# Performance work log

Measured on AMD Instinct MI355X. Metric: run time of the kernel, lower is better.

Reference implementation:

```python
import jax, jax.numpy as jnp
import numpy as np

B, L, DM = 16, 1024, 128
DK = DV = 32
HF, HG, HC, HP, HT, HA = 2, 2, 2, 2, 1, 2  # full, log, local, prob, FFT, auto heads
MA = 25          # series_decomp moving average window
WIN = 32         # local attention causal window
EPS = 1e-5
SCALE = float(1.0 / np.sqrt(DK))

_i = np.arange(L)[:, None]
_j = np.arange(L)[None, :]
_d = _i - _j
# log-sparse: attend to self and keys at power-of-two causal distances
LOG_MASK = jnp.asarray((_d == 0) | ((_d > 0) & ((_d & (_d - 1)) == 0)))
LOC_MASK = jnp.asarray((_d >= 0) & (_d < WIN))
# ProbSparse (Informer, factor=5): fixed sample indices, u = U_part
_U = min(int(5 * np.ceil(np.log(L))), L)
PROB_IDX = jnp.asarray(np.random.RandomState(0).randint(0, L, size=(L, _U)))
AUTO_K = int(np.log(L))  # AutoCorrelation factor=1


def _cconv(x, w, b, pad):
    # x [B,L,DM] -> conv over time in NCH layout; pad-left = causal (Conv pad=2 + Chomp1d(2))
    y = jax.lax.conv_general_dilated(x.swapaxes(1, 2), w, (1,), [(pad, 0)],
                                     dimension_numbers=('NCH', 'OIH', 'NCH'))
    return y + b[None, :, None]


def _heads(y, H, d):
    # faithful to torch: .view(B, L, H, d) applied to [B, C, L] conv output (memory reinterpret)
    return y.reshape(y.shape[0], L, H, d)


def _qkv(xq, xk, xv, wq, bq, wk, bk, wv, bv, H):
    Q = _heads(_cconv(xq, wq, bq, 2), H, DK)
    K = _heads(_cconv(xk, wk, bk, 2), H, DK)
    V = _heads(_cconv(xv, wv, bv, 0), H, DV)
    return Q, K, V


def _attn(Q, K, V, mask=None):
    s = jnp.einsum('blhe,bshe->bhls', Q, K) * SCALE
    if mask is not None:
        s = jnp.where(mask, s, -1e9)
    return jnp.einsum('bhls,bshd->blhd', jax.nn.softmax(s, axis=-1), V)


def _prob_attn(Q, K, V):
    q, k, v = Q.swapaxes(1, 2), K.swapaxes(1, 2), V.swapaxes(1, 2)  # [B,H,L,D]
    Ks = k[:, :, PROB_IDX]                                  # [B,H,L,U,D] sampled keys
    qk = jnp.einsum('bhld,bhlud->bhlu', q, Ks)
    M = qk.max(-1) - qk.sum(-1) / L                         # sparsity measure
    top = jax.lax.top_k(M, _U)[1]                           # [B,H,u] active queries
    qr = jnp.take_along_axis(q, top[..., None], axis=2)
    sc = jnp.einsum('bhud,bhsd->bhus', qr, k) * SCALE
    cu = jnp.einsum('bhus,bhsd->bhud', jax.nn.softmax(sc, -1), v)
    ctx = jnp.broadcast_to(v.mean(axis=2, keepdims=True), v.shape)  # lazy queries get mean(V)
    bi = jnp.arange(v.shape[0])[:, None, None]
    hi = jnp.arange(v.shape[1])[None, :, None]
    return ctx.at[bi, hi, top].set(cu).swapaxes(1, 2)


def _auto_corr(Q, K, V):
    q = Q.transpose(0, 2, 3, 1)  # [B,H,E,L]
    k = K.transpose(0, 2, 3, 1)
    v = V.transpose(0, 2, 3, 1)
    corr = jnp.fft.irfft(jnp.fft.rfft(q, axis=-1) * jnp.conj(jnp.fft.rfft(k, axis=-1)), n=L, axis=-1)
    mv = corr.mean(axis=1).mean(axis=1)                     # [B,L] mean over heads+channels
    idx = jax.lax.top_k(mv.mean(axis=0), AUTO_K)[1]         # shared top-k delays
    w = jax.nn.softmax(mv[:, idx], axis=-1)                 # [B,k]
    tt = jnp.arange(L)
    agg = jnp.zeros_like(v)
    for i in range(AUTO_K):
        agg = agg + v[..., (tt + idx[i]) % L] * w[:, i][:, None, None, None]
    return agg.transpose(0, 3, 1, 2)                        # [B,L,H,E]


def _mavg(x, k):
    # replicate-padded moving average (Autoformer series_decomp) via cumsum
    p = (k - 1) // 2
    xp = jnp.concatenate([jnp.repeat(x[:, :1], p, axis=1), x, jnp.repeat(x[:, -1:], p, axis=1)], axis=1)
    cs = jnp.cumsum(xp, axis=1)
    cs = jnp.concatenate([jnp.zeros_like(cs[:, :1]), cs], axis=1)
    return (cs[:, k:] - cs[:, :-k]) / k


def _forward(fl):
    (iq, ik, iv,
     wqf, bqf, wkf, bkf, wvf, bvf,
     wqg, bqg, wkg, bkg, wvg, bvg,
     wql, bql, wkl, bkl, wvl, bvl,
     wqp, bqp, wkp, bkp, wvp, bvp,
     wqa, bqa, wka, bka, wva, bva,
     wfft, bfft, wap, bap, was, bas, wfc) = fl
    ctx = []
    Q, K, V = _qkv(iq, ik, iv, wqf, bqf, wkf, bkf, wvf, bvf, HF)
    ctx.append(_attn(Q, K, V))
    Q, K, V = _qkv(iq, ik, iv, wqg, bqg, wkg, bkg, wvg, bvg, HG)
    ctx.append(_attn(Q, K, V, LOG_MASK))
    Q, K, V = _qkv(iq, ik, iv, wql, bql, wkl, bkl, wvl, bvl, HC)
    ctx.append(_attn(Q, K, V, LOC_MASK))
    Q, K, V = _qkv(iq, ik, iv, wqp, bqp, wkp, bkp, wvp, bvp, HP)
    ctx.append(_prob_attn(Q, K, V))
    cf = jnp.fft.fft(iq, axis=1).real                       # FFT branch
    ctx.append((cf @ wfft + bfft).reshape(B, L, HT, DV))
    Q, K, V = _qkv(iq, ik, iv, wqa, bqa, wka, bka, wva, bva, HA)
    ca = _auto_corr(Q, K, V).reshape(B, L, HA * DV) @ wap + bap
    ca = iq + ca                                            # residual (dropout=eval identity)
    ca = ca - _mavg(ca, MA)                                 # seasonal part of series_decomp
    ctx.append((ca @ was + bas).reshape(B, L, HA, DV))
    c = jnp.concatenate(ctx, axis=2).reshape(B, L, -1)
    out = c @ wfc + iq
    mu = out.mean(-1, keepdims=True)
    var = out.var(-1, keepdims=True)                        # fresh LayerNorm: weight=1, bias=0
    return (out - mu) / jnp.sqrt(var + EPS)


def setup_inputs() -> dict:
    ks = iter(jax.random.split(jax.random.key(0), 64))
    def n(shape, s=0.02):
        return jax.random.normal(next(ks), shape, dtype=jnp.float32) * s
    d = {}
    d['input_Q'] = jax.random.normal(next(ks), (B, L, DM), dtype=jnp.float32)
    d['input_K'] = jax.random.normal(next(ks), (B, L, DM), dtype=jnp.float32)
    d['input_V'] = jax.random.normal(next(ks), (B, L, DM), dtype=jnp.float32)
    for nm, H in [('full', HF), ('log', HG), ('loc', HC), ('prob', HP), ('auto', HA)]:
        d['wq_' + nm] = n((DK * H, DM, 3)); d['bq_' + nm] = n((DK * H,))
        d['wk_' + nm] = n((DK * H, DM, 3)); d['bk_' + nm] = n((DK * H,))
        d['wv_' + nm] = n((DV * H, DM, 1)); d['bv_' + nm] = n((DV * H,))
    d['w_fft'] = n((DM, DV * HT)); d['b_fft'] = n((DV * HT,))
    d['w_aproj'] = n((DV * HA, DM)); d['b_aproj'] = n((DM,))
    d['w_asize'] = n((DM, DV * HA)); d['b_asize'] = n((DV * HA,))
    d['w_fc'] = n(((HF + HG + HC + HP + HT + HA) * DV, DM))
    return d


def reference(input_Q, input_K, input_V, wq_full, bq_full, wk_full, bk_full, wv_full, bv_full, wq_log, bq_log, wk_log, bk_log, wv_log, bv_log, wq_loc, bq_loc, wk_loc, bk_loc, wv_loc, bv_loc, wq_prob, bq_prob, wk_prob, bk_prob, wv_prob, bv_prob, wq_auto, bq_auto, wk_auto, bk_auto, wv_auto, bv_auto, w_fft, b_fft, w_aproj, b_aproj, w_asize, b_asize, w_fc):
    return _forward((input_Q, input_K, input_V, wq_full, bq_full, wk_full, bk_full, wv_full, bv_full, wq_log, bq_log, wk_log, bk_log, wv_log, bv_log, wq_loc, bq_loc, wk_loc, bk_loc, wv_loc, bv_loc, wq_prob, bq_prob, wk_prob, bk_prob, wv_prob, bv_prob, wq_auto, bq_auto, wk_auto, bk_auto, wv_auto, bv_auto, w_fft, b_fft, w_aproj, b_aproj, w_asize, b_asize, w_fc))
```

## Files before the change

### kernel.cpp

```cpp
#include <hip/hip_runtime.h>
#include <hip/hip_bf16.h>
#include <math.h>

#define B_   16
#define L_   1024
#define SCALE_ 0.17677669529663687f

__global__ void mt_kernel(int* __restrict__ pidx) {
  __shared__ unsigned int mt[624];
  int tid = threadIdx.x;
  if (tid == 0) {
    unsigned int s = 0u;
    for (int i = 0; i < 624; ++i) {
      mt[i] = s;
      s = 1812433253u * (s ^ (s >> 30)) + (unsigned)(i + 1);
    }
  }
  __syncthreads();
  const unsigned int HI = 0x80000000u, LO = 0x7fffffffu, MM = 0x9908b0dfu;
  for (int blk = 0; blk < 58; ++blk) {
    unsigned int n0 = 0, n1 = 0, n2 = 0, old623 = 0;
    bool a0 = tid < 227, a2 = tid < 169;
    if (a0) {
      unsigned int y0 = (mt[tid] & HI) | (mt[tid + 1] & LO);
      n0 = mt[tid + 397] ^ (y0 >> 1) ^ ((y0 & 1u) ? MM : 0u);
      unsigned int y1 = (mt[tid + 227] & HI) | (mt[tid + 228] & LO);
      n1 = n0 ^ (y1 >> 1) ^ ((y1 & 1u) ? MM : 0u);
      if (a2) {
        unsigned int y2 = (mt[tid + 454] & HI) | (mt[tid + 455] & LO);
        n2 = n1 ^ (y2 >> 1) ^ ((y2 & 1u) ? MM : 0u);
      }
      if (tid == 169) old623 = mt[623];
    }
    __syncthreads();
    if (a0) {
      mt[tid] = n0;
      mt[tid + 227] = n1;
      if (a2) mt[tid + 454] = n2;
    }
    __syncthreads();
    if (tid == 169) {
      unsigned int y = (old623 & HI) | (mt[0] & LO);
      mt[623] = n1 ^ (y >> 1) ^ ((y & 1u) ? MM : 0u);
    }
    __syncthreads();
    for (int i = tid; i < 624; i += 256) {
      int g = blk * 624 + i;
      if (g < 35840) {
        unsigned int y = mt[i];
        y ^= y >> 11;
        y ^= (y << 7) & 0x9d2c5680u;
        y ^= (y << 15) & 0xefc60000u;
        y ^= y >> 18;
        pidx[g] = (int)(y & 1023u);
      }
    }
  }
}

__device__ __forceinline__ void conv_body(const float* __restrict__ x,
                                          const float* __restrict__ w,
                                          const float* __restrict__ bias,
                                          float* __restrict__ out,
                                          float* smem, int b, int t0, int tid, int is1) {
  int c = tid & 63, tt0 = (tid >> 6) * 8;
  float acc[8];
  float bvv = bias[c];
  #pragma unroll
  for (int j = 0; j < 8; ++j) acc[j] = bvv;
  if (!is1) {
    float* xs = smem;
    float* ws = smem + 4352;
    for (int i = tid; i < 34 * 128; i += 256) {
      int r = i >> 7, d = i & 127;
      int t = t0 - 2 + r;
      xs[r * 128 + d] = (t >= 0) ? x[(size_t)b * 131072 + (size_t)t * 128 + d] : 0.0f;
    }
    for (int dc = 0; dc < 128; dc += 16) {
      __syncthreads();
      {
        int row = tid >> 2, sub = tid & 3;
        const float* wsrc = w + row * 384 + dc * 3 + sub * 12;
        float* wdst = ws + row * 49 + sub * 12;
        #pragma unroll
        for (int k = 0; k < 12; ++k) wdst[k] = wsrc[k];
      }
      __syncthreads();
      #pragma unroll
      for (int dl = 0; dl < 16; dl += 4) {
        int d0 = dc + dl;
        float4 xr[10];
        #pragma unroll
        for (int r = 0; r < 10; ++r) xr[r] = *(const float4*)&xs[(tt0 + r) * 128 + d0];
        float wreg[12];
        #pragma unroll
        for (int jj = 0; jj < 12; ++jj) wreg[jj] = ws[c * 49 + dl * 3 + jj];
        #pragma unroll
        for (int j = 0; j < 8; ++j) {
          float a = acc[j];
          #pragma unroll
          for (int k = 0; k < 3; ++k) {
            float4 xv4 = xr[j + k];
            a = fmaf(wreg[0 + k], xv4.x, a);
            a = fmaf(wreg[3 + k], xv4.y, a);
            a = fmaf(wreg[6 + k], xv4.z, a);
            a = fmaf(wreg[9 + k], xv4.w, a);
          }
          acc[j] = a;
        }
      }
    }
  } else {
    float* xs = smem;
    float* ws = smem + 4096;
    for (int i = tid; i < 32 * 128; i += 256) {
      int r = i >> 7, d = i & 127;
      xs[r * 128 + d] = x[(size_t)b * 131072 + (size_t)(t0 + r) * 128 + d];
    }
    for (int dc = 0; dc < 128; dc += 32) {
      __syncthreads();
      {
        int row = tid >> 2, sub = tid & 3;
        const float* wsrc = w + row * 128 + dc + sub * 8;
        float* wdst = ws + row * 33 + sub * 8;
        #pragma unroll
        for (int k = 0; k < 8; ++k) wdst[k] = wsrc[k];
      }
      __syncthreads();
      #pragma unroll
      for (int dl = 0; dl < 32; dl += 4) {
        int d0 = dc + dl;
        float w0 = ws[c * 33 + dl], w1 = ws[c * 33 + dl + 1];
        float w2 = ws[c * 33 + dl + 2], w3 = ws[c * 33 + dl + 3];
        #pragma unroll
        for (int j = 0; j < 8; ++j) {
          float4 xv4 = *(const float4*)&xs[(tt0 + j) * 128 + d0];
          float a = acc[j];
          a = fmaf(w0, xv4.x, a);
          a = fmaf(w1, xv4.y, a);
          a = fmaf(w2, xv4.z, a);
          a = fmaf(w3, xv4.w, a);
          acc[j] = a;
        }
      }
    }
  }
  float* op = out + (size_t)b * 65536 + (size_t)c * 1024 + t0 + tt0;
  #pragma unroll
  for (int j = 0; j < 8; ++j) op[j] = acc[j];
}

__global__ __launch_bounds__(256, 4)
void qkv_conv_kernel(const float* __restrict__ xq, const float* __restrict__ xk,
                     const float* __restrict__ xv,
                     const float* __restrict__ wq, const float* __restrict__ bq,
                     const float* __restrict__ wk, const float* __restrict__ bk,
                     const float* __restrict__ wv, const float* __restrict__ bv,
                     float* __restrict__ qo, float* __restrict__ ko,
                     float* __restrict__ vo) {
  __shared__ float smem[7488];
  int which = blockIdx.z;
  const float* x = (which == 0) ? xq : (which == 1) ? xk : xv;
  const float* w = (which == 0) ? wq : (which == 1) ? wk : wv;
  const float* bias = (which == 0) ? bq : (which == 1) ? bk : bv;
  float* out = (which == 0) ? qo : (which == 1) ? ko : vo;
  conv_body(x, w, bias, out, smem, blockIdx.y, blockIdx.x * 32, threadIdx.x, which == 2);
}

struct ConvArgs {
  const float* x[3];
  const float* w[15];
  const float* bia[15];
  float* outbase;
};
__global__ __launch_bounds__(256, 4)
void qkv_conv_all(ConvArgs a) {
  __shared__ float smem[7488];
  int z = blockIdx.z;
  int which = z % 3;
  float* out = a.outbase + (size_t)z * 1048576;
  conv_body(a.x[which], a.w[z], a.bia[z], out, smem, blockIdx.y, blockIdx.x * 32,
            threadIdx.x, which == 2);
}

__global__ __launch_bounds__(256, 2)
void attn_full_part(const float* __restrict__ Q, const float* __restrict__ K,
                    const float* __restrict__ V, float* __restrict__ part,
                    int stile, int nstage) {
  __shared__ float Ks[128][32];
  __shared__ float Vs[128][32];
  int bh = blockIdx.z, b = bh >> 1, h = bh & 1;
  int l = blockIdx.x * 256 + threadIdx.x;
  int s0 = blockIdx.y * stile;
  const float* Kb = K + (size_t)b * 65536 + h * 32;
  const float* Vb = V + (size_t)b * 65536 + h * 32;
  const float* Qb = Q + (size_t)b * 65536 + h * 32 + (size_t)l * 64;
  float q[32];
  #pragma unroll
  for (int i = 0; i < 8; ++i) {
    float4 v4 = ((const float4*)Qb)[i];
    q[4*i] = v4.x; q[4*i+1] = v4.y; q[4*i+2] = v4.z; q[4*i+3] = v4.w;
  }
  float o[32];
  #pragma unroll
  for (int d = 0; d < 32; ++d) o[d] = 0.0f;
  float ssum = 0.0f;
  for (int st = 0; st < nstage; ++st) {
    __syncthreads();
    int sb = s0 + st * 128;
    for (int i = threadIdx.x; i < 1024; i += 256) {
      int r = i >> 3, d4 = i & 7;
      ((float4*)&Ks[r][0])[d4] = *(const float4*)(Kb + (size_t)(sb + r) * 64 + d4 * 4);
      ((float4*)&Vs[r][0])[d4] = *(const float4*)(Vb + (size_t)(sb + r) * 64 + d4 * 4);
    }
    __syncthreads();
    for (int s = 0; s < 128; s += 2) {
      const float4* kp0 = (const float4*)&Ks[s][0];
      const float4* kp1 = (const float4*)&Ks[s + 1][0];
      float a0 = 0, a1 = 0, a2 = 0, a3 = 0;
      float c0 = 0, c1 = 0, c2 = 0, c3 = 0;
      #pragma unroll
      for (int i = 0; i < 8; ++i) {
        float4 k0 = kp0[i], k1 = kp1[i];
        float qx = q[4*i], qy = q[4*i+1], qz = q[4*i+2], qw = q[4*i+3];
        a0 = fmaf(qx, k0.x, a0); a1 = fmaf(qy, k0.y, a1);
        a2 = fmaf(qz, k0.z, a2); a3 = fmaf(qw, k0.w, a3);
        c0 = fmaf(qx, k1.x, c0); c1 = fmaf(qy, k1.y, c1);
        c2 = fmaf(qz, k1.z, c2); c3 = fmaf(qw, k1.w, c3);
      }
      float p0 = __expf(((a0 + a1) + (a2 + a3)) * SCALE_);
      float p1 = __expf(((c0 + c1) + (c2 + c3)) * SCALE_);
      ssum += p0 + p1;
      const float4* vp0 = (const float4*)&Vs[s][0];
      const float4* vp1 = (const float4*)&Vs[s + 1][0];
      #pragma unroll
      for (int i = 0; i < 8; ++i) {
        float4 v0 = vp0[i], v1 = vp1[i];
        o[4*i]   = fmaf(p0, v0.x, fmaf(p1, v1.x, o[4*i]));
        o[4*i+1] = fmaf(p0, v0.y, fmaf(p1, v1.y, o[4*i+1]));
        o[4*i+2] = fmaf(p0, v0.z, fmaf(p1, v1.z, o[4*i+2]));
        o[4*i+3] = fmaf(p0, v0.w, fmaf(p1, v1.w, o[4*i+3]));
      }
    }
  }
  float* pp = part + (((size_t)bh * gridDim.y + blockIdx.y) * 1024 + l) * 36;
  #pragma unroll
  for (int i = 0; i < 8; ++i)
    ((float4*)pp)[i] = make_float4(o[4*i], o[4*i+1], o[4*i+2], o[4*i+3]);
  pp[32] = ssum;
}

__global__ void attn_full_comb(const float* __restrict__ part, float* __restrict__ cbuf,
                               int nsplit) {
  int idx = blockIdx.x * 128 + threadIdx.x;
  int bh = idx >> 10, l = idx & 1023;
  int b = bh >> 1, h = bh & 1;
  float S = 0.0f;
  float o[32];
  #pragma unroll
  for (int d = 0; d < 32; ++d) o[d] = 0.0f;
  for (int j = 0; j < nsplit; ++j) {
    const float* pp = part + (((size_t)bh * nsplit + j) * 1024 + l) * 36;
    S += pp[32];
    #pragma unroll
    for (int i = 0; i < 8; ++i) {
      float4 v4 = ((const float4*)pp)[i];
      o[4*i] += v4.x; o[4*i+1] += v4.y; o[4*i+2] += v4.z; o[4*i+3] += v4.w;
    }
  }
  float inv = 1.0f / S;
  float* cc = cbuf + ((size_t)b * 1024 + l) * 352 + 0 + h * 32;
  #pragma unroll
  for (int d = 0; d < 32; ++d) cc[d] = o[d] * inv;
}

__global__ void attn_log_kernel(const float* __restrict__ Q, const float* __restrict__ K,
                                const float* __restrict__ V, float* __restrict__ cbuf) {
  int idx = blockIdx.x * 128 + threadIdx.x;
  int bh = idx >> 10, l = idx & 1023;
  int b = bh >> 1, h = bh & 1;
  const float* Qb = Q + (size_t)b * 65536 + h * 32;
  const float* Kb = K + (size_t)b * 65536 + h * 32;
  const float* Vb = V + (size_t)b * 65536 + h * 32;
  float q[32];
  #pragma unroll
  for (int i = 0; i < 8; ++i) {
    float4 v4 = ((const float4*)(Qb + (size_t)l * 64))[i];
    q[4*i] = v4.x; q[4*i+1] = v4.y; q[4*i+2] = v4.z; q[4*i+3] = v4.w;
  }
  float o[32];
  #pragma unroll
  for (int d = 0; d < 32; ++d) o[d] = 0.0f;
  float ssum = 0.0f;
  #pragma unroll
  for (int j = 0; j < 11; ++j) {
    int off = (j == 0) ? 0 : (1 << (j - 1));
    if (off <= l) {
      int s = l - off;
      const float4* kp = (const float4*)(Kb + (size_t)s * 64);
      float a0 = 0, a1 = 0, a2 = 0, a3 = 0;
      #pragma unroll
      for (int i = 0; i < 8; ++i) {
        float4 kv = kp[i];
        a0 = fmaf(q[4*i], kv.x, a0);
        a1 = fmaf(q[4*i+1], kv.y, a1);
        a2 = fmaf(q[4*i+2], kv.z, a2);
        a3 = fmaf(q[4*i+3], kv.w, a3);
      }
      float p = __expf(((a0 + a1) + (a2 + a3)) * SCALE_);
      ssum += p;
      const float4* vp = (const float4*)(Vb + (size_t)s * 64);
      #pragma unroll
      for (int i = 0; i < 8; ++i) {
        float4 vv = vp[i];
        o[4*i]   = fmaf(p, vv.x, o[4*i]);
        o[4*i+1] = fmaf(p, vv.y, o[4*i+1]);
        o[4*i+2] = fmaf(p, vv.z, o[4*i+2]);
        o[4*i+3] = fmaf(p, vv.w, o[4*i+3]);
      }
    }
  }
  float inv = 1.0f / ssum;
  float* cc = cbuf + ((size_t)b * 1024 + l) * 352 + 64 + h * 32;
  #pragma unroll
  for (int d = 0; d < 32; ++d) cc[d] = o[d] * inv;
}

__global__ void attn_loc_kernel(const float* __restrict__ Q, const float* __restrict__ K,
                                const float* __restrict__ V, float* __restrict__ cbuf) {
  int idx = blockIdx.x * 128 + threadIdx.x;
  int bh = idx >> 10, l = idx & 1023;
  int b = bh >> 1, h = bh & 1;
  const float* Qb = Q + (size_t)b * 65536 + h * 32;
  const float* Kb = K + (size_t)b * 65536 + h * 32;
  const float* Vb = V + (size_t)b * 65536 + h * 32;
  float q[32];
  #pragma unroll
  for (int i = 0; i < 8; ++i) {
    float4 v4 = ((const float4*)(Qb + (size_t)l * 64))[i];
    q[4*i] = v4.x; q[4*i+1] = v4.y; q[4*i+2] = v4.z; q[4*i+3] = v4.w;
  }
  float o[32];
  #pragma unroll
  for (int d = 0; d < 32; ++d) o[d] = 0.0f;
  float ssum = 0.0f;
  int jlo = (l >= 31) ? 0 : (31 - l);
  for (int j = jlo; j < 32; ++j) {
    int s = l - 31 + j;
    const float4* kp = (const float4*)(Kb + (size_t)s * 64);
    float a0 = 0, a1 = 0, a2 = 0, a3 = 0;
    #pragma unroll
    for (int i = 0; i < 8; ++i) {
      float4 kv = kp[i];
      a0 = fmaf(q[4*i], kv.x, a0);
      a1 = fmaf(q[4*i+1], kv.y, a1);
      a2 = fmaf(q[4*i+2], kv.z, a2);
      a3 = fmaf(q[4*i+3], kv.w, a3);
    }
    float p = __expf(((a0 + a1) + (a2 + a3)) * SCALE_);
    ssum += p;
    const float4* vp = (const float4*)(Vb + (size_t)s * 64);
    #pragma unroll
    for (int i = 0; i < 8; ++i) {
      float4 vv = vp[i];
      o[4*i]   = fmaf(p, vv.x, o[4*i]);
      o[4*i+1] = fmaf(p, vv.y, o[4*i+1]);
      o[4*i+2] = fmaf(p, vv.z, o[4*i+2]);
      o[4*i+3] = fmaf(p, vv.w, o[4*i+3]);
    }
  }
  float inv = 1.0f / ssum;
  float* cc = cbuf + ((size_t)b * 1024 + l) * 352 + 128 + h * 32;
  #pragma unroll
  for (int d = 0; d < 32; ++d) cc[d] = o[d] * inv;
}

__global__ void prob_m_kernel(const float* __restrict__ Q, const float* __restrict__ K,
                              const int* __restrict__ pidx, float* __restrict__ Mbuf) {
  int idx = blockIdx.x * 128 + threadIdx.x;
  int bh = idx >> 10, l = idx & 1023;
  int b = bh >> 1, h = bh & 1;
  const float* Qb = Q + (size_t)b * 65536 + h * 32;
  const float* Kb = K + (size_t)b * 65536 + h * 32;
  float q[32];
  #pragma unroll
  for (int i = 0; i < 8; ++i) {
    float4 v4 = ((const float4*)(Qb + (size_t)l * 64))[i];
    q[4*i] = v4.x; q[4*i+1] = v4.y; q[4*i+2] = v4.z; q[4*i+3] = v4.w;
  }
  float mx = -1e30f, sm = 0.0f;
  for (int u = 0; u < 35; ++u) {
    int ki = pidx[l * 35 + u];
    const float4* kp = (const float4*)(Kb + (size_t)ki * 64);
    float a0 = 0, a1 = 0, a2 = 0, a3 = 0;
    #pragma unroll
    for (int i = 0; i < 8; ++i) {
      float4 kv = kp[i];
      a0 = fmaf(q[4*i], kv.x, a0);
      a1 = fmaf(q[4*i+1], kv.y, a1);
      a2 = fmaf(q[4*i+2], kv.z, a2);
      a3 = fmaf(q[4*i+3], kv.w, a3);
    }
    float s = (a0 + a1) + (a2 + a3);
    mx = fmaxf(mx, s);
    sm += s;
  }
  Mbuf[(size_t)bh * 1024 + l] = mx - sm * (1.0f / 1024.0f);
}

__global__ void top35_kernel(const float* __restrict__ Mbuf, int* __restrict__ sel) {
  int bh = blockIdx.x;
  int lane = threadIdx.x;
  float v[16];
  const float* Mb = Mbuf + (size_t)bh * 1024 + lane * 16;
  #pragma unroll
  for (int k = 0; k < 16; ++k) v[k] = Mb[k];
  for (int it = 0; it < 35; ++it) {
    float bv = -1e30f; int bi = 0;
    #pragma unroll
    for (int k = 0; k < 16; ++k)
      if (v[k] > bv) { bv = v[k]; bi = k; }
    int gidx = lane * 16 + bi;
    #pragma unroll
    for (int off = 32; off > 0; off >>= 1) {
      float ov = __shfl_down(bv, off, 64);
      int og = __shfl_down(gidx, off, 64);
      if (ov > bv || (ov == bv && og < gidx)) { bv = ov; gidx = og; }
    }
    gidx = __shfl(gidx, 0, 64);
    if (lane == 0) sel[bh * 35 + it] = gidx;
    if ((gidx >> 4) == lane) {
      int kk = gidx & 15;
      #pragma unroll
      for (int k = 0; k < 16; ++k)
        if (k == kk) v[k] = -1e30f;
    }
  }
}

__global__ void prob_fill_kernel(const float* __restrict__ V, float* __restrict__ cbuf) {
  __shared__ float red[256];
  __shared__ float vm[32];
  int bh = blockIdx.x, b = bh >> 1, h = bh & 1;
  int tid = threadIdx.x;
  int d = tid & 31, ch = tid >> 5;
  const float* Vb = V + (size_t)b * 65536 + h * 32;
  float s = 0.0f;
  for (int ss = ch * 128; ss < ch * 128 + 128; ++ss) s += Vb[(size_t)ss * 64 + d];
  red[tid] = s;
  __syncthreads();
  if (ch == 0) {
    float t = 0.0f;
    for (int c = 0; c < 8; ++c) t += red[c * 32 + d];
    vm[d] = t * (1.0f / 1024.0f);
  }
  __syncthreads();
  for (int i = tid; i < 1024 * 32; i += 256) {
    int l = i >> 5, dd = i & 31;
    cbuf[((size_t)b * 1024 + l) * 352 + 192 + h * 32 + dd] = vm[dd];
  }
}

__global__ void prob_part_kernel(const float* __restrict__ Q, const float* __restrict__ K,
                                 const float* __restrict__ V, const int* __restrict__ sel,
                                 float* __restrict__ ppart) {
  int bh = blockIdx.y, b = bh >> 1, h = bh & 1;
  int sc0 = blockIdx.x * 64;
  int u = threadIdx.x;
  int uu = (u < 35) ? u : 34;
  int l = sel[bh * 35 + uu];
  const float* Qb = Q + (size_t)b * 65536 + h * 32;
  const float* Kb = K + (size_t)b * 65536 + h * 32;
  const float* Vb = V + (size_t)b * 65536 + h * 32;
  float q[32];
  #pragma unroll
  for (int i = 0; i < 8; ++i) {
    float4 v4 = ((const float4*)(Qb + (size_t)l * 64))[i];
    q[4*i] = v4.x; q[4*i+1] = v4.y; q[4*i+2] = v4.z; q[4*i+3] = v4.w;
  }
  float o[32];
  #pragma unroll
  for (int dd = 0; dd < 32; ++dd) o[dd] = 0.0f;
  float ssum = 0.0f;
  for (int s = sc0; s < sc0 + 64; ++s) {
    const float4* kp = (const float4*)(Kb + (size_t)s * 64);
    float a0 = 0, a1 = 0, a2 = 0, a3 = 0;
    #pragma unroll
    for (int i = 0; i < 8; ++i) {
      float4 kv = kp[i];
      a0 = fmaf(q[4*i], kv.x, a0);
      a1 = fmaf(q[4*i+1], kv.y, a1);
      a2 = fmaf(q[4*i+2], kv.z, a2);
      a3 = fmaf(q[4*i+3], kv.w, a3);
    }
    float p = __expf(((a0 + a1) + (a2 + a3)) * SCALE_);
    ssum += p;
    const float4* vp = (const float4*)(Vb + (size_t)s * 64);
    #pragma unroll
    for (int i = 0; i < 8; ++i) {
      float4 vv = vp[i];
      o[4*i]   = fmaf(p, vv.x, o[4*i]);
      o[4*i+1] = fmaf(p, vv.y, o[4*i+1]);
      o[4*i+2] = fmaf(p, vv.z, o[4*i+2]);
      o[4*i+3] = fmaf(p, vv.w, o[4*i+3]);
    }
  }
  if (u < 35) {
    float* pp = ppart + (((size_t)bh * 16 + blockIdx.x) * 35 + u) * 36;
    #pragma unroll
    for (int i = 0; i < 8; ++i)
      ((float4*)pp)[i] = make_float4(o[4*i], o[4*i+1], o[4*i+2], o[4*i+3]);
    pp[32] = ssum;
  }
}

__global__ void prob_comb_kernel(const float* __restrict__ ppart, const int* __restrict__ sel,
                                 float* __restrict__ cbuf) {
  int t = blockIdx.x * 64 + threadIdx.x;
  if (t >= 32 * 35) return;
  int bh = t / 35, u = t % 35;
  int b = bh >> 1, h = bh & 1;
  int l = sel[bh * 35 + u];
  float S = 0.0f;
  float o[32];
  #pragma unroll
  for (int d = 0; d < 32; ++d) o[d] = 0.0f;
  for (int j = 0; j < 16; ++j) {
    const float* pp = ppart + (((size_t)bh * 16 + j) * 35 + u) * 36;
    S += pp[32];
    #pragma unroll
    for (int i = 0; i < 8; ++i) {
      float4 v4 = ((const float4*)pp)[i];
      o[4*i] += v4.x; o[4*i+1] += v4.y; o[4*i+2] += v4.z; o[4*i+3] += v4.w;
    }
  }
  float inv = 1.0f / S;
  float* cc = cbuf + ((size_t)b * 1024 + l) * 352 + 192 + h * 32;
  #pragma unroll
  for (int d = 0; d < 32; ++d) cc[d] = o[d] * inv;
}

__global__ void auto_mv_part(const float* __restrict__ Qa, const float* __restrict__ Ka,
                             float* __restrict__ part) {
  __shared__ float qs[1280];
  int c = blockIdx.x, tq = blockIdx.y, b = blockIdx.z;
  int tid = threadIdx.x;
  int tau0 = tq * 256;
  const float* Qb = Qa + (size_t)b * 65536 + (size_t)c * 1024;
  const float* Kb = Ka + (size_t)b * 65536 + (size_t)c * 1024;
  for (int i = tid; i < 1280; i += 256) qs[i] = Qb[(tau0 + i) & 1023];
  __syncthreads();
  float a0 = 0, a1 = 0, a2 = 0, a3 = 0;
  for (int t = 0; t < 1024; t += 8) {
    float4 k0 = *(const float4*)(Kb + t);
    float4 k1 = *(const float4*)(Kb + t + 4);
    const float* qp = &qs[t + tid];
    a0 = fmaf(k0.x, qp[0], a0);
    a1 = fmaf(k0.y, qp[1], a1);
    a2 = fmaf(k0.z, qp[2], a2);
    a3 = fmaf(k0.w, qp[3], a3);
    a0 = fmaf(k1.x, qp[4], a0);
    a1 = fmaf(k1.y, qp[5], a1);
    a2 = fmaf(k1.z, qp[6], a2);
    a3 = fmaf(k1.w, qp[7], a3);
  }
  part[(((size_t)b * 64 + c) << 10) + tau0 + tid] = (a0 + a1) + (a2 + a3);
}

__global__ void auto_mv_reduce(const float* __restrict__ part, float* __restrict__ mv) {
  int idx = blockIdx.x * 256 + threadIdx.x;
  int b = idx >> 10, tau = idx & 1023;
  float s = 0.0f;
  for (int c = 0; c < 64; ++c) s += part[(((size_t)b * 64 + c) << 10) + tau];
  mv[(size_t)b * 1024 + tau] = s * (1.0f / 64.0f);
}

__global__ void auto_top6_kernel(const float* __restrict__ mv, int* __restrict__ idx6,
                                 float* __restrict__ w6) {
  __shared__ int id6s[6];
  int lane = threadIdx.x;
  float v[16];
  #pragma unroll
  for (int k = 0; k < 16; ++k) {
    int i = lane * 16 + k;
    float s = 0.0f;
    for (int b = 0; b < 16; ++b) s += mv[(size_t)b * 1024 + i];
    v[k] = s;
  }
  for (int it = 0; it < 6; ++it) {
    float bv = -1e30f; int bi = 0;
    #pragma unroll
    for (int k = 0; k < 16; ++k)
      if (v[k] > bv) { bv = v[k]; bi = k; }
    int gidx = lane * 16 + bi;
    #pragma unroll
    for (int off = 32; off > 0; off >>= 1) {
      float ov = __shfl_down(bv, off, 64);
      int og = __shfl_down(gidx, off, 64);
      if (ov > bv || (ov == bv && og < gidx)) { bv = ov; gidx = og; }
    }
    gidx = __shfl(gidx, 0, 64);
    if (lane == 0) { idx6[it] = gidx; id6s[it] = gidx; }
    if ((gidx >> 4) == lane) {
      int kk = gidx & 15;
      #pragma unroll
      for (int k = 0; k < 16; ++k)
        if (k == kk) v[k] = -1e30f;
    }
  }
  __syncthreads();
  if (lane < 16) {
    int b = lane;
    float vals[6]; float mx = -1e30f;
    #pragma unroll
    for (int j = 0; j < 6; ++j) { vals[j] = mv[(size_t)b * 1024 + id6s[j]]; mx = fmaxf(mx, vals[j]); }
    float s = 0.0f;
    #pragma unroll
    for (int j = 0; j < 6; ++j) { vals[j] = __expf(vals[j] - mx); s += vals[j]; }
    #pragma unroll
    for (int j = 0; j < 6; ++j) w6[b * 6 + j] = vals[j] / s;
  }
}

__global__ void auto_agg_kernel(const float* __restrict__ Va, const float* __restrict__ iq,
                                const float* __restrict__ wap, const float* __restrict__ bap,
                                const int* __restrict__ idx6, const float* __restrict__ w6,
                                float* __restrict__ ca) {
  __shared__ float aggs[16][64];
  __shared__ float w6s[6];
  __shared__ int id6[6];
  int b = blockIdx.y, t0 = blockIdx.x * 16;
  int tid = threadIdx.x;
  if (tid < 6) { w6s[tid] = w6[b * 6 + tid]; id6[tid] = idx6[tid]; }
  __syncthreads();
  const float* Vb = Va + (size_t)b * 65536;
  for (int i = tid; i < 1024; i += 256) {
    int tl = i >> 6, c = i & 63;
    int t = t0 + tl;
    float s = 0.0f;
    #pragma unroll
    for (int j = 0; j < 6; ++j)
      s += w6s[j] * Vb[(size_t)((t + id6[j]) & 1023) * 64 + c];
    aggs[tl][c] = s;
  }
  __syncthreads();
  int dm = tid & 127, tp = tid >> 7;
  float acc[8];
  #pragma unroll
  for (int r = 0; r < 8; ++r) {
    int t = t0 + tp * 8 + r;
    acc[r] = bap[dm] + iq[((size_t)b * 1024 + t) * 128 + dm];
  }
  for (int c = 0; c < 64; ++c) {
    float wv = wap[c * 128 + dm];
    #pragma unroll
    for (int r = 0; r < 8; ++r) acc[r] += aggs[tp * 8 + r][c] * wv;
  }
  #pragma unroll
  for (int r = 0; r < 8; ++r)
    ca[((size_t)b * 1024 + t0 + tp * 8 + r) * 128 + dm] = acc[r];
}

__global__ void auto_ma_kernel(const float* __restrict__ ca, const float* __restrict__ was,
                               const float* __restrict__ bas, float* __restrict__ cbuf) {
  __shared__ float cas[40][128];
  __shared__ float diff[16][128];
  int b = blockIdx.y, t0 = blockIdx.x * 16;
  int tid = threadIdx.x;
  for (int i = tid; i < 40 * 128; i += 256) {
    int r = i >> 7, d = i & 127;
    int t = t0 - 12 + r;
    t = (t < 0) ? 0 : ((t > 1023) ? 1023 : t);
    cas[r][d] = ca[((size_t)b * 1024 + t) * 128 + d];
  }
  __syncthreads();
  int d = tid & 127, hf = tid >> 7;
  int tl0 = hf * 8;
  float s = 0.0f;
  #pragma unroll
  for (int w = 0; w < 25; ++w) s += cas[tl0 + w][d];
  #pragma unroll
  for (int k = 0; k < 8; ++k) {
    int tl = tl0 + k;
    diff[tl][d] = cas[tl + 12][d] - s * (1.0f / 25.0f);
    if (k < 7) s += cas[tl + 25][d] - cas[tl][d];
  }
  __syncthreads();
  int j = tid & 63, tq = tid >> 6;
  float acc[4];
  #pragma unroll
  for (int r = 0; r < 4; ++r) acc[r] = bas[j];
  for (int dd = 0; dd < 128; ++dd) {
    float wv = was[dd * 64 + j];
    #pragma unroll
    for (int r = 0; r < 4; ++r) acc[r] += diff[tq * 4 + r][dd] * wv;
  }
  #pragma unroll
  for (int r = 0; r < 4; ++r)
    cbuf[((size_t)b * 1024 + t0 + tq * 4 + r) * 352 + 288 + j] = acc[r];
}

__global__ void fftY_kernel(const float* __restrict__ x, const float* __restrict__ wfft,
                            float* __restrict__ Y) {
  __shared__ float xs[64][128];
  __shared__ float ws[32][129];
  int b = blockIdx.y, t0 = blockIdx.x * 64;
  int tid = threadIdx.x;
  for (int i = tid; i < 64 * 128; i += 256) {
    int r = i >> 7, d = i & 127;
    xs[r][d] = x[(size_t)b * 131072 + (size_t)(t0 + r) * 128 + d];
  }
  for (int i = tid; i < 4096; i += 256) {
    int d = i >> 5, j = i & 31;
    ws[j][d] = wfft[i];
  }
  __syncthreads();
  int j = tid & 31, tt0 = (tid >> 5) * 8;
  float acc[8];
  #pragma unroll
  for (int r = 0; r < 8; ++r) acc[r] = 0.0f;
  for (int d0 = 0; d0 < 128; d0 += 4) {
    float w0 = ws[j][d0], w1 = ws[j][d0 + 1], w2 = ws[j][d0 + 2], w3 = ws[j][d0 + 3];
    #pragma unroll
    for (int r = 0; r < 8; ++r) {
      float4 xv = *(const float4*)&xs[tt0 + r][d0];
      float a = acc[r];
      a = fmaf(w0, xv.x, a);
      a = fmaf(w1, xv.y, a);
      a = fmaf(w2, xv.z, a);
      a = fmaf(w3, xv.w, a);
      acc[r] = a;
    }
  }
  #pragma unroll
  for (int r = 0; r < 8; ++r)
    Y[((size_t)b * 1024 + t0 + tt0 + r) * 32 + j] = acc[r];
}

__global__ void fftT_kernel(const float* __restrict__ Y, const float* __restrict__ bfft,
                            float* __restrict__ cbuf) {
  __shared__ float ys[256 * 32];
  __shared__ float altred[8][32];
  int b = blockIdx.y, fbase = blockIdx.x * 64;
  int tid = threadIdx.x;
  int fi = tid & 31, jg = tid >> 5, j0 = jg * 4;
  int f0 = fbase + fi * 2;
  const float TWO_PI_N = 6.283185307179586476925f / 1024.0f;
  float ca0, sa0, ca1, sa1;
  sincosf(TWO_PI_N * (float)f0, &sa0, &ca0);
  sincosf(TWO_PI_N * (float)(f0 + 1), &sa1, &ca1);
  float cr0 = 1.0f, ci0 = 0.0f, cr1 = 1.0f, ci1 = 0.0f;
  float4 acc0 = make_float4(0.f, 0.f, 0.f, 0.f);
  float4 acc1 = make_float4(0.f, 0.f, 0.f, 0.f);
  bool do512 = (blockIdx.x == 0);
  int aj = tid & 31, arow = tid >> 5;
  float alt = 0.0f;
  for (int chk = 0; chk < 4; ++chk) {
    __syncthreads();
    const float4* Yp = (const float4*)(Y + ((size_t)b * 1024 + chk * 256) * 32);
    for (int i = tid; i < 2048; i += 256) ((float4*)ys)[i] = Yp[i];
    __syncthreads();
    for (int tl = 0; tl < 256; ++tl) {
      float4 yv = *(const float4*)&ys[tl * 32 + j0];
      acc0.x = fmaf(cr0, yv.x, acc0.x);
      acc0.y = fmaf(cr0, yv.y, acc0.y);
      acc0.z = fmaf(cr0, yv.z, acc0.z);
      acc0.w = fmaf(cr0, yv.w, acc0.w);
      acc1.x = fmaf(cr1, yv.x, acc1.x);
      acc1.y = fmaf(cr1, yv.y, acc1.y);
      acc1.z = fmaf(cr1, yv.z, acc1.z);
      acc1.w = fmaf(cr1, yv.w, acc1.w);
      float nr0 = cr0 * ca0 - ci0 * sa0;
      float ni0 = cr0 * sa0 + ci0 * ca0;
      cr0 = nr0; ci0 = ni0;
      float nr1 = cr1 * ca1 - ci1 * sa1;
      float ni1 = cr1 * sa1 + ci1 * ca1;
      cr1 = nr1; ci1 = ni1;
    }
    if (do512) {
      int tb = arow * 32;
      #pragma unroll 8
      for (int k = 0; k < 32; ++k) {
        float y = ys[(tb + k) * 32 + aj];
        alt += ((tb + k) & 1) ? -y : y;
      }
    }
  }
  float b0 = bfft[j0], b1 = bfft[j0 + 1], b2 = bfft[j0 + 2], b3 = bfft[j0 + 3];
  float* cc0 = cbuf + ((size_t)b * 1024 + f0) * 352 + 256 + j0;
  cc0[0] = acc0.x + b0; cc0[1] = acc0.y + b1; cc0[2] = acc0.z + b2; cc0[3] = acc0.w + b3;
  float* cc1 = cbuf + ((size_t)b * 1024 + f0 + 1) * 352 + 256 + j0;
  cc1[0] = acc1.x + b0; cc1[1] = acc1.y + b1; cc1[2] = acc1.z + b2; cc1[3] = acc1.w + b3;
  if (f0 > 0) {
    float* cm0 = cbuf + ((size_t)b * 1024 + (1024 - f0)) * 352 + 256 + j0;
    cm0[0] = acc0.x + b0; cm0[1] = acc0.y + b1; cm0[2] = acc0.z + b2; cm0[3] = acc0.w + b3;
  }
  {
    float* cm1 = cbuf + ((size_t)b * 1024 + (1024 - f0 - 1)) * 352 + 256 + j0;
    cm1[0] = acc1.x + b0; cm1[1] = acc1.y + b1; cm1[2] = acc1.z + b2; cm1[3] = acc1.w + b3;
  }
  if (do512) {
    altred[arow][aj] = alt;
    __syncthreads();
    if (tid < 32) {
      float s = 0.0f;
      #pragma unroll
      for (int r = 0; r < 8; ++r) s += altred[r][tid];
      cbuf[((size_t)b * 1024 + 512) * 352 + 256 + tid] = s + bfft[tid];
    }
  }
}

__global__ void fc_ln_kernel(const float* __restrict__ cbuf, const float* __restrict__ wfc,
                             const float* __restrict__ iq, float* __restrict__ out) {
  __shared__ float cs[16][352];
  __shared__ float os[16][128];
  int b = blockIdx.y, t0 = blockIdx.x * 16;
  int tid = threadIdx.x;
  for (int i = tid; i < 16 * 352; i += 256) {
    int r = i / 352, col = i % 352;
    cs[r][col] = cbuf[((size_t)b * 1024 + t0 + r) * 352 + col];
  }
  __syncthreads();
  int j = tid & 127, half = tid >> 7;
  float acc[8];
  #pragma unroll
  for (int k = 0; k < 8; ++k)
    acc[k] = iq[((size_t)b * 1024 + t0 + half * 8 + k) * 128 + j];
  for (int i = 0; i < 352; ++i) {
    float wv = wfc[i * 128 + j];
    #pragma unroll
    for (int k = 0; k < 8; ++k) acc[k] += cs[half * 8 + k][i] * wv;
  }
  #pragma unroll
  for (int k = 0; k < 8; ++k) os[half * 8 + k][j] = acc[k];
  __syncthreads();
  int wid = tid >> 6, lane = tid & 63;
  for (int rr = 0; rr < 4; ++rr) {
    int r = wid * 4 + rr;
    float x0 = os[r][lane], x1 = os[r][lane + 64];
    float s1 = x0 + x1;
    float s2 = x0 * x0 + x1 * x1;
    #pragma unroll
    for (int k = 32; k > 0; k >>= 1) {
      s1 += __shfl_xor(s1, k, 64);
      s2 += __shfl_xor(s2, k, 64);
    }
    float mean = s1 * (1.0f / 128.0f);
    float var = s2 * (1.0f / 128.0f) - mean * mean;
    float rstd = 1.0f / sqrtf(var + 1e-5f);
    float* op = out + ((size_t)b * 1024 + t0 + r) * 128;
    op[lane] = (x0 - mean) * rstd;
    op[lane + 64] = (x1 - mean) * rstd;
  }
}

extern "C" void kernel_launch(void* const* d_in, const int* in_sizes, int n_in,
                              void* d_out, int out_size, void* d_ws, size_t ws_size,
                              hipStream_t stream) {
  (void)in_sizes; (void)n_in; (void)out_size;
  const float* inQ = (const float*)d_in[0];
  const float* inK = (const float*)d_in[1];
  const float* inV = (const float*)d_in[2];
  const float *wq[5], *bq[5], *wk[5], *bk[5], *wv[5], *bv[5];
  for (int br = 0; br < 5; ++br) {
    wq[br] = (const float*)d_in[3 + br * 6 + 0];
    bq[br] = (const float*)d_in[3 + br * 6 + 1];
    wk[br] = (const float*)d_in[3 + br * 6 + 2];
    bk[br] = (const float*)d_in[3 + br * 6 + 3];
    wv[br] = (const float*)d_in[3 + br * 6 + 4];
    bv[br] = (const float*)d_in[3 + br * 6 + 5];
  }
  const float* wfft = (const float*)d_in[33];
  const float* bfft = (const float*)d_in[34];
  const float* wap  = (const float*)d_in[35];
  const float* bap  = (const float*)d_in[36];
  const float* was  = (const float*)d_in[37];
  const float* bas  = (const float*)d_in[38];
  const float* wfc  = (const float*)d_in[39];
  float* out = (float*)d_out;

  bool mega = ws_size >= (size_t)128 * 1024 * 1024;
  int nsplit = (ws_size >= (size_t)76 * 1024 * 1024) ? 8 : 4;
  int stile = 1024 / nsplit;
  int nstage = stile / 128;

  char* wsb = (char*)d_ws;
  size_t off = 0;
  auto alloc = [&](size_t bytes) -> void* {
    void* p = wsb + off;
    off += (bytes + 255) & ~(size_t)255;
    return p;
  };
  int*   pidx = (int*)  alloc((size_t)35840 * 4);
  float* qkvall = (float*)alloc((size_t)(mega ? 15 : 3) * 1048576 * 4);
  float* cbuf = (float*)alloc((size_t)16 * 1024 * 352 * 4);
  float* fpart = (float*)alloc((size_t)32 * nsplit * 1024 * 36 * 4);
  float* Mbuf = (float*)alloc((size_t)32 * 1024 * 4);
  int*   sel  = (int*)  alloc((size_t)32 * 35 * 4);
  float* mvb  = (float*)alloc((size_t)16 * 1024 * 4);
  int*   idx6 = (int*)  alloc(64);
  float* w6   = (float*)alloc((size_t)16 * 6 * 4);
  float* ppart = fpart;
  float* cab   = fpart;
  float* mpart = (float*)((char*)fpart + (size_t)8 * 1024 * 1024);
  float* Ybuf  = (float*)((char*)fpart + (size_t)12 * 1024 * 1024);

  mt_kernel<<<1, 256, 0, stream>>>(pidx);

  if (mega) {
    ConvArgs ca;
    ca.x[0] = inQ; ca.x[1] = inK; ca.x[2] = inV;
    for (int br = 0; br < 5; ++br) {
      ca.w[br * 3 + 0] = wq[br]; ca.bia[br * 3 + 0] = bq[br];
      ca.w[br * 3 + 1] = wk[br]; ca.bia[br * 3 + 1] = bk[br];
      ca.w[br * 3 + 2] = wv[br]; ca.bia[br * 3 + 2] = bv[br];
    }
    ca.outbase = qkvall;
    qkv_conv_all<<<dim3(32, 16, 15), 256, 0, stream>>>(ca);
  }
  auto bufs = [&](int br, float*& qb, float*& kb, float*& vb) {
    int bi = mega ? br : 0;
    qb = qkvall + (size_t)(bi * 3 + 0) * 1048576;
    kb = qkvall + (size_t)(bi * 3 + 1) * 1048576;
    vb = qkvall + (size_t)(bi * 3 + 2) * 1048576;
  };
  auto conv_branch = [&](int br, float* qb, float* kb, float* vb) {
    if (!mega)
      qkv_conv_kernel<<<dim3(32, 16, 3), 256, 0, stream>>>(
          inQ, inK, inV, wq[br], bq[br], wk[br], bk[br], wv[br], bv[br], qb, kb, vb);
  };
  float *qb, *kb, *vb;

  bufs(0, qb, kb, vb);
  conv_branch(0, qb, kb, vb);
  attn_full_part<<<dim3(4, nsplit, 32), 256, 0, stream>>>(qb, kb, vb, fpart, stile, nstage);
  attn_full_comb<<<256, 128, 0, stream>>>(fpart, cbuf, nsplit);

  bufs(1, qb, kb, vb);
  conv_branch(1, qb, kb, vb);
  attn_log_kernel<<<256, 128, 0, stream>>>(qb, kb, vb, cbuf);

  bufs(2, qb, kb, vb);
  conv_branch(2, qb, kb, vb);
  attn_loc_kernel<<<256, 128, 0, stream>>>(qb, kb, vb, cbuf);

  bufs(3, qb, kb, vb);
  conv_branch(3, qb, kb, vb);
  prob_m_kernel<<<256, 128, 0, stream>>>(qb, kb, pidx, Mbuf);
  top35_kernel<<<32, 64, 0, stream>>>(Mbuf, sel);
  prob_fill_kernel<<<32, 256, 0, stream>>>(vb, cbuf);
  prob_part_kernel<<<dim3(16, 32), 64, 0, stream>>>(qb, kb, vb, sel, ppart);
  prob_comb_kernel<<<18, 64, 0, stream>>>(ppart, sel, cbuf);

  bufs(4, qb, kb, vb);
  conv_branch(4, qb, kb, vb);
  auto_mv_part<<<dim3(64, 4, 16), 256, 0, stream>>>(qb, kb, mpart);
  auto_mv_reduce<<<64, 256, 0, stream>>>(mpart, mvb);
  auto_top6_kernel<<<1, 64, 0, stream>>>(mvb, idx6, w6);
  auto_agg_kernel<<<dim3(64, 16), 256, 0, stream>>>(vb, inQ, wap, bap, idx6, w6, cab);
  auto_ma_kernel<<<dim3(64, 16), 256, 0, stream>>>(cab, was, bas, cbuf);

  fftY_kernel<<<dim3(16, 16), 256, 0, stream>>>(inQ, wfft, Ybuf);
  fftT_kernel<<<dim3(8, 16), 256, 0, stream>>>(Ybuf, bfft, cbuf);

  fc_ln_kernel<<<dim3(64, 16), 256, 0, stream>>>(cbuf, wfc, inQ, out);
}
```

Baseline: 764.5 us.

## Enlarge conv register tile to two channels and 64 timesteps per block

The causal QKV convolution now has each thread compute two output channels (cp and cp+32) for 8 timesteps, and each block covers 64 timesteps instead of 32. Every x value loaded from shared memory is reused for twice as many FMAs. Weights are read as float4 with a padded stride, outputs are written as float4, and the grid is halved along time. The larger shared tile and doubled accumulators lower the occupancy target from 4 to 3 blocks per CU and leave fewer blocks in the grid.

```diff
diff --git a/kernel.cpp b/kernel.cpp
--- a/kernel.cpp
+++ b/kernel.cpp
@@ -63,15 +63,17 @@
                                           const float* __restrict__ bias,
                                           float* __restrict__ out,
                                           float* smem, int b, int t0, int tid, int is1) {
-  int c = tid & 63, tt0 = (tid >> 6) * 8;
-  float acc[8];
-  float bvv = bias[c];
-  #pragma unroll
-  for (int j = 0; j < 8; ++j) acc[j] = bvv;
+  int cp = tid & 31;
+  int tg = tid >> 5;
+  int tt0 = tg * 8;
+  float acc0[8], acc1[8];
+  float b0v = bias[cp], b1v = bias[cp + 32];
+  #pragma unroll
+  for (int j = 0; j < 8; ++j) { acc0[j] = b0v; acc1[j] = b1v; }
   if (!is1) {
     float* xs = smem;
-    float* ws = smem + 4352;
-    for (int i = tid; i < 34 * 128; i += 256) {
+    float* ws = smem + 8448;
+    for (int i = tid; i < 66 * 128; i += 256) {
       int r = i >> 7, d = i & 127;
       int t = t0 - 2 + r;
       xs[r * 128 + d] = (t >= 0) ? x[(size_t)b * 131072 + (size_t)t * 128 + d] : 0.0f;
@@ -81,7 +83,7 @@
       {
         int row = tid >> 2, sub = tid & 3;
         const float* wsrc = w + row * 384 + dc * 3 + sub * 12;
-        float* wdst = ws + row * 49 + sub * 12;
+        float* wdst = ws + row * 52 + sub * 12;
         #pragma unroll
         for (int k = 0; k < 12; ++k) wdst[k] = wsrc[k];
       }
@@ -92,28 +94,39 @@
         float4 xr[10];
         #pragma unroll
         for (int r = 0; r < 10; ++r) xr[r] = *(const float4*)&xs[(tt0 + r) * 128 + d0];
-        float wreg[12];
-        #pragma unroll
-        for (int jj = 0; jj < 12; ++jj) wreg[jj] = ws[c * 49 + dl * 3 + jj];
+        float4 wa0 = *(const float4*)&ws[cp * 52 + dl * 3];
+        float4 wa1 = *(const float4*)&ws[cp * 52 + dl * 3 + 4];
+        float4 wa2 = *(const float4*)&ws[cp * 52 + dl * 3 + 8];
+        float4 wb0 = *(const float4*)&ws[(cp + 32) * 52 + dl * 3];
+        float4 wb1 = *(const float4*)&ws[(cp + 32) * 52 + dl * 3 + 4];
+        float4 wb2 = *(const float4*)&ws[(cp + 32) * 52 + dl * 3 + 8];
+        float w0r[12] = {wa0.x, wa0.y, wa0.z, wa0.w, wa1.x, wa1.y, wa1.z, wa1.w,
+                         wa2.x, wa2.y, wa2.z, wa2.w};
+        float w1r[12] = {wb0.x, wb0.y, wb0.z, wb0.w, wb1.x, wb1.y, wb1.z, wb1.w,
+                         wb2.x, wb2.y, wb2.z, wb2.w};
         #pragma unroll
         for (int j = 0; j < 8; ++j) {
-          float a = acc[j];
+          float a0 = acc0[j], a1 = acc1[j];
           #pragma unroll
           for (int k = 0; k < 3; ++k) {
-            float4 xv4 = xr[j + k];
-            a = fmaf(wreg[0 + k], xv4.x, a);
-            a = fmaf(wreg[3 + k], xv4.y, a);
-            a = fmaf(wreg[6 + k], xv4.z, a);
-            a = fmaf(wreg[9 + k], xv4.w, a);
+            float4 xv = xr[j + k];
+            a0 = fmaf(w0r[0 + k], xv.x, a0);
+            a0 = fmaf(w0r[3 + k], xv.y, a0);
+            a0 = fmaf(w0r[6 + k], xv.z, a0);
+            a0 = fmaf(w0r[9 + k], xv.w, a0);
+            a1 = fmaf(w1r[0 + k], xv.x, a1);
+            a1 = fmaf(w1r[3 + k], xv.y, a1);
+            a1 = fmaf(w1r[6 + k], xv.z, a1);
+            a1 = fmaf(w1r[9 + k], xv.w, a1);
           }
-          acc[j] = a;
+          acc0[j] = a0; acc1[j] = a1;
         }
       }
     }
   } else {
     float* xs = smem;
-    float* ws = smem + 4096;
-    for (int i = tid; i < 32 * 128; i += 256) {
+    float* ws = smem + 8192;
+    for (int i = tid; i < 64 * 128; i += 256) {
       int r = i >> 7, d = i & 127;
       xs[r * 128 + d] = x[(size_t)b * 131072 + (size_t)(t0 + r) * 128 + d];
     }
@@ -122,7 +135,7 @@
       {
         int row = tid >> 2, sub = tid & 3;
         const float* wsrc = w + row * 128 + dc + sub * 8;
-        float* wdst = ws + row * 33 + sub * 8;
+        float* wdst = ws + row * 36 + sub * 8;
         #pragma unroll
         for (int k = 0; k < 8; ++k) wdst[k] = wsrc[k];
       }
@@ -130,27 +143,34 @@
       #pragma unroll
       for (int dl = 0; dl < 32; dl += 4) {
         int d0 = dc + dl;
-        float w0 = ws[c * 33 + dl], w1 = ws[c * 33 + dl + 1];
-        float w2 = ws[c * 33 + dl + 2], w3 = ws[c * 33 + dl + 3];
+        float4 wv0 = *(const float4*)&ws[cp * 36 + dl];
+        float4 wv1 = *(const float4*)&ws[(cp + 32) * 36 + dl];
         #pragma unroll
         for (int j = 0; j < 8; ++j) {
-          float4 xv4 = *(const float4*)&xs[(tt0 + j) * 128 + d0];
-          float a = acc[j];
-          a = fmaf(w0, xv4.x, a);
-          a = fmaf(w1, xv4.y, a);
-          a = fmaf(w2, xv4.z, a);
-          a = fmaf(w3, xv4.w, a);
-          acc[j] = a;
+          float4 xv = *(const float4*)&xs[(tt0 + j) * 128 + d0];
+          float a0 = acc0[j], a1 = acc1[j];
+          a0 = fmaf(wv0.x, xv.x, a0);
+          a0 = fmaf(wv0.y, xv.y, a0);
+          a0 = fmaf(wv0.z, xv.z, a0);
+          a0 = fmaf(wv0.w, xv.w, a0);
+          a1 = fmaf(wv1.x, xv.x, a1);
+          a1 = fmaf(wv1.y, xv.y, a1);
+          a1 = fmaf(wv1.z, xv.z, a1);
+          a1 = fmaf(wv1.w, xv.w, a1);
+          acc0[j] = a0; acc1[j] = a1;
         }
       }
     }
   }
-  float* op = out + (size_t)b * 65536 + (size_t)c * 1024 + t0 + tt0;
-  #pragma unroll
-  for (int j = 0; j < 8; ++j) op[j] = acc[j];
-}
-
-__global__ __launch_bounds__(256, 4)
+  float* op0 = out + (size_t)b * 65536 + (size_t)cp * 1024 + t0 + tt0;
+  float* op1 = out + (size_t)b * 65536 + (size_t)(cp + 32) * 1024 + t0 + tt0;
+  *(float4*)op0 = make_float4(acc0[0], acc0[1], acc0[2], acc0[3]);
+  *(float4*)(op0 + 4) = make_float4(acc0[4], acc0[5], acc0[6], acc0[7]);
+  *(float4*)op1 = make_float4(acc1[0], acc1[1], acc1[2], acc1[3]);
+  *(float4*)(op1 + 4) = make_float4(acc1[4], acc1[5], acc1[6], acc1[7]);
+}
+
+__global__ __launch_bounds__(256, 3)
 void qkv_conv_kernel(const float* __restrict__ xq, const float* __restrict__ xk,
                      const float* __restrict__ xv,
                      const float* __restrict__ wq, const float* __restrict__ bq,
@@ -158,13 +178,13 @@
                      const float* __restrict__ wv, const float* __restrict__ bv,
                      float* __restrict__ qo, float* __restrict__ ko,
                      float* __restrict__ vo) {
-  __shared__ float smem[7488];
+  __shared__ float smem[11776];
   int which = blockIdx.z;
   const float* x = (which == 0) ? xq : (which == 1) ? xk : xv;
   const float* w = (which == 0) ? wq : (which == 1) ? wk : wv;
   const float* bias = (which == 0) ? bq : (which == 1) ? bk : bv;
   float* out = (which == 0) ? qo : (which == 1) ? ko : vo;
-  conv_body(x, w, bias, out, smem, blockIdx.y, blockIdx.x * 32, threadIdx.x, which == 2);
+  conv_body(x, w, bias, out, smem, blockIdx.y, blockIdx.x * 64, threadIdx.x, which == 2);
 }
 
 struct ConvArgs {
@@ -173,13 +193,13 @@
   const float* bia[15];
   float* outbase;
 };
-__global__ __launch_bounds__(256, 4)
+__global__ __launch_bounds__(256, 3)
 void qkv_conv_all(ConvArgs a) {
-  __shared__ float smem[7488];
+  __shared__ float smem[11776];
   int z = blockIdx.z;
   int which = z % 3;
   float* out = a.outbase + (size_t)z * 1048576;
-  conv_body(a.x[which], a.w[z], a.bia[z], out, smem, blockIdx.y, blockIdx.x * 32,
+  conv_body(a.x[which], a.w[z], a.bia[z], out, smem, blockIdx.y, blockIdx.x * 64,
             threadIdx.x, which == 2);
 }
 
@@ -917,7 +937,7 @@
       ca.w[br * 3 + 2] = wv[br]; ca.bia[br * 3 + 2] = bv[br];
     }
     ca.outbase = qkvall;
-    qkv_conv_all<<<dim3(32, 16, 15), 256, 0, stream>>>(ca);
+    qkv_conv_all<<<dim3(16, 16, 15), 256, 0, stream>>>(ca);
   }
   auto bufs = [&](int br, float*& qb, float*& kb, float*& vb) {
     int bi = mega ? br : 0;
@@ -927,7 +947,7 @@
   };
   auto conv_branch = [&](int br, float* qb, float* kb, float* vb) {
     if (!mega)
-      qkv_conv_kernel<<<dim3(32, 16, 3), 256, 0, stream>>>(
+      qkv_conv_kernel<<<dim3(16, 16, 3), 256, 0, stream>>>(
           inQ, inK, inV, wq[br], bq[br], wk[br], bk[br], wv[br], bv[br], qb, kb, vb);
   };
   float *qb, *kb, *vb;
```

Result: faster. 727.7 us (-4.8%).
